# Kernel tuning notes

Measured on AMD Instinct MI355X. Metric: run time of the kernel, lower is better.

Reference implementation:

```python
import jax, jax.numpy as jnp
import numpy as np

B, N, F = 4, 3000, 128

def setup_inputs() -> dict:
    key = jax.random.key(0)
    k1, k2, k3, k4 = jax.random.split(key, 4)
    x = jax.random.normal(k1, (B, N, F), dtype=jnp.float32)
    adj = jax.random.uniform(k2, (B, N, N), dtype=jnp.float32)
    h0 = jax.random.normal(k3, (B, N, F), dtype=jnp.float32)
    stdv = 1.0 / np.sqrt(F)
    theta = jax.random.uniform(k4, (F, F), dtype=jnp.float32, minval=-stdv, maxval=stdv)
    return {
        "x": x, "adj": adj, "h0": h0, "theta": theta,
        "lamda": jnp.float32(0.5), "alpha": jnp.float32(0.1), "l": 4,
    }

def _normalize_adj(adj):
    # add self loops, then D^{-1/2} A D^{-1/2} via elementwise row/col scaling
    # (same math as diag-embed + inverse + two bmms in the original)
    n = adj.shape[1]
    adj = adj + jnp.eye(n, dtype=adj.dtype)
    deg = jnp.sum(adj, axis=2)                      # [B, N]
    d_inv_sqrt = jax.lax.rsqrt(deg)                 # [B, N]
    return d_inv_sqrt[:, :, None] * adj * d_inv_sqrt[:, None, :]

def reference(x, adj, h0, theta, lamda, alpha, l):
    adj_n = _normalize_adj(adj)
    beta = jnp.log(lamda / l + 1.0)
    hi = jnp.einsum('bnm,bmf->bnf', adj_n, x)       # aggregation
    support = (1.0 - alpha) * hi + alpha * h0       # variant=False path
    r = support
    out = beta * jnp.einsum('bnf,fg->bng', support, theta) + (1.0 - beta) * r
    return out
```

## Files before the change

kernel.cpp:

```cpp
#include <hip/hip_runtime.h>
#include <hip/hip_bf16.h>
#include <math.h>

#define BB 4
#define NN 3000
#define FF 128
#define NKC 96
#define NIT 188
#define TS  532

typedef __bf16 bf16x8 __attribute__((ext_vector_type(8)));
typedef __bf16 bf16x4 __attribute__((ext_vector_type(4)));
typedef __bf16 bf16x8a __attribute__((ext_vector_type(8), aligned(8)));
typedef __bf16 bf16x4a __attribute__((ext_vector_type(4), aligned(4)));
typedef float  f32x4  __attribute__((ext_vector_type(4)));


__global__ __launch_bounds__(256) void k_degpk(const float* __restrict__ adj,
                                               float* __restrict__ dis,
                                               __bf16* __restrict__ apk) {
    const int b = blockIdx.y, it = blockIdx.x;
    const int i0 = it * 16;
    const int t = threadIdx.x, w = t >> 6, l = t & 63;
    const int m = l & 15, q = l >> 4;
    const int irow = i0 + m;
    const bool rv = irow < NN;
    const float* arow = adj + ((size_t)b * NN + irow) * NN;
    __bf16* apt = apk + ((size_t)(b * NIT + it) * NKC) * 512 + l * 8;

    float rsum = 0.f;
    for (int kc = w; kc < NKC; kc += 4) {
        int c0 = kc * 32 + q * 8;
        float4 u = {0.f, 0.f, 0.f, 0.f}, v = {0.f, 0.f, 0.f, 0.f};
        if (rv && c0 + 8 <= NN) {
            u = *(const float4*)(arow + c0);
            v = *(const float4*)(arow + c0 + 4);
        }
        rsum += (u.x + u.y) + (u.z + u.w) + (v.x + v.y) + (v.z + v.w);
        bf16x8 s;
        s[0] = (__bf16)u.x; s[1] = (__bf16)u.y; s[2] = (__bf16)u.z; s[3] = (__bf16)u.w;
        s[4] = (__bf16)v.x; s[5] = (__bf16)v.y; s[6] = (__bf16)v.z; s[7] = (__bf16)v.w;
        *(bf16x8*)(apt + (size_t)kc * 512) = s;
    }
    rsum += __shfl_xor(rsum, 16, 64);
    rsum += __shfl_xor(rsum, 32, 64);
    __shared__ float ssum[4][16];
    if (q == 0) ssum[w][m] = rsum;
    __syncthreads();
    if (t < 16 && i0 + t < NN) {
        float tot = ssum[0][t] + ssum[1][t] + ssum[2][t] + ssum[3][t] + 1.0f;
        dis[b * NN + i0 + t] = 1.0f / sqrtf(tot);
    }
}

__global__ __launch_bounds__(256) void k_aggs(const __bf16* __restrict__ apk,
                                              const __bf16* __restrict__ xpk,
                                              const __bf16* __restrict__ thpk,
                                              const float* __restrict__ x,
                                              const float* __restrict__ h0,
                                              const float* __restrict__ dis,
                                              float* __restrict__ out,
                                              const float* __restrict__ alpha_p,
                                              const float* __restrict__ lamda_p,
                                              const int* __restrict__ l_p) {
    __shared__ __bf16 stile[16][140];
    const int id = blockIdx.x;
    const int b  = (id >> 1) & 3;
    const int it = (id >> 3) * 2 + (id & 1);
    const int i0 = it * 16;
    const int t  = threadIdx.x, w = t >> 6, l = t & 63;
    const int m  = l & 15, quad = l >> 4;
    const int n0 = w * 32;
    const __bf16* A0 = apk + ((size_t)(b * NIT + it) * NKC) * 512 + l * 8;
    const __bf16* B0 = xpk + ((size_t)(b * 8 + 2 * w) * NKC) * 512 + l * 8;
    const __bf16* B1 = B0 + (size_t)NKC * 512;
    f32x4 acc0 = {0.f, 0.f, 0.f, 0.f};
    f32x4 acc1 = {0.f, 0.f, 0.f, 0.f};

    #pragma unroll 8
    for (int kc = 0; kc < NKC; ++kc) {
        bf16x8 a  = *(const bf16x8*)(A0 + (size_t)kc * 512);
        bf16x8 b0 = *(const bf16x8*)(B0 + (size_t)kc * 512);
        bf16x8 b1 = *(const bf16x8*)(B1 + (size_t)kc * 512);
        acc0 = __builtin_amdgcn_mfma_f32_16x16x32_bf16(a, b0, acc0, 0, 0, 0);
        acc1 = __builtin_amdgcn_mfma_f32_16x16x32_bf16(a, b1, acc1, 0, 0, 0);
    }

    const float alpha = *alpha_p;
    const float beta  = logf(*lamda_p / (float)(*l_p) + 1.0f);
    float s0v[4], s1v[4];
    #pragma unroll
    for (int r = 0; r < 4; ++r) {
        int row  = quad * 4 + r;
        int irow = i0 + row;
        float s0 = 0.f, s1 = 0.f;
        if (irow < NN) {
            float  di   = dis[b * NN + irow];
            size_t base = ((size_t)b * NN + irow) * FF;
            int c0 = n0 + m, c1 = n0 + 16 + m;
            s0 = (1.f - alpha) * (di * acc0[r] + di * di * x[base + c0]) + alpha * h0[base + c0];
            s1 = (1.f - alpha) * (di * acc1[r] + di * di * x[base + c1]) + alpha * h0[base + c1];
        }
        s0v[r] = s0; s1v[r] = s1;
        stile[row][n0 + m]      = (__bf16)s0;
        stile[row][n0 + 16 + m] = (__bf16)s1;
    }
    __syncthreads();
    f32x4 o0 = {0.f, 0.f, 0.f, 0.f};
    f32x4 o1 = {0.f, 0.f, 0.f, 0.f};
    const __bf16* T0 = thpk + (size_t)(2 * w * 4) * 512 + l * 8;
    const __bf16* T1 = T0 + 4 * 512;
    #pragma unroll
    for (int kc = 0; kc < 4; ++kc) {
        bf16x4a alo = *(const bf16x4a*)&stile[m][kc * 32 + quad * 8];
        bf16x4a ahi = *(const bf16x4a*)&stile[m][kc * 32 + quad * 8 + 4];
        bf16x8 a = __builtin_shufflevector(alo, ahi, 0, 1, 2, 3, 4, 5, 6, 7);
        bf16x8 tb0 = *(const bf16x8*)(T0 + (size_t)kc * 512);
        bf16x8 tb1 = *(const bf16x8*)(T1 + (size_t)kc * 512);
        o0 = __builtin_amdgcn_mfma_f32_16x16x32_bf16(a, tb0, o0, 0, 0, 0);
        o1 = __builtin_amdgcn_mfma_f32_16x16x32_bf16(a, tb1, o1, 0, 0, 0);
    }
    const float omb = 1.f - beta;
    #pragma unroll
    for (int r = 0; r < 4; ++r) {
        int irow = i0 + quad * 4 + r;
        if (irow < NN) {
            size_t base = ((size_t)b * NN + irow) * FF;
            out[base + n0 + m]      = beta * o0[r] + omb * s0v[r];
            out[base + n0 + 16 + m] = beta * o1[r] + omb * s1v[r];
        }
    }
}


__global__ __launch_bounds__(256) void k_xpk(const float* __restrict__ x,
                                             const float* __restrict__ dis,
                                             __bf16* __restrict__ xpk) {
    int b  = blockIdx.y, kc = blockIdx.x;
    int t  = threadIdx.x, w = t >> 6, l = t & 63;
    int m  = l & 15, q = l >> 4;
    #pragma unroll
    for (int h = 0; h < 2; ++h) {
        int nt = w + h * 4;
        int f  = nt * 16 + m;
        bf16x8 v;
        #pragma unroll
        for (int j = 0; j < 8; ++j) {
            int k = kc * 32 + q * 8 + j;
            float val = 0.f;
            if (k < NN) val = dis[b * NN + k] * x[((size_t)b * NN + k) * FF + f];
            v[j] = (__bf16)val;
        }
        *(bf16x8*)(xpk + ((size_t)(b * 8 + nt) * NKC + kc) * 512 + l * 8) = v;
    }
}

__global__ __launch_bounds__(256) void k_thpk(const float* __restrict__ theta,
                                              __bf16* __restrict__ thpk) {
    int kc = blockIdx.x;
    int t  = threadIdx.x, w = t >> 6, l = t & 63;
    int m  = l & 15, q = l >> 4;
    #pragma unroll
    for (int h = 0; h < 2; ++h) {
        int nt = w + h * 4;
        bf16x8 v;
        #pragma unroll
        for (int j = 0; j < 8; ++j) {
            int k = kc * 32 + q * 8 + j;
            v[j] = (__bf16)theta[k * FF + nt * 16 + m];
        }
        *(bf16x8*)(thpk + ((size_t)(nt * 4 + kc)) * 512 + l * 8) = v;
    }
}


__global__ __launch_bounds__(256) void k_deg(const float* __restrict__ adj,
                                             float* __restrict__ dis) {
    int wid  = (blockIdx.x * 256 + threadIdx.x) >> 6;
    int lane = threadIdx.x & 63;
    if (wid >= BB * NN) return;
    const float4* row = (const float4*)(adj + (size_t)wid * NN);
    float s = 0.f;
    for (int c = lane; c < NN / 4; c += 64) {
        float4 v = row[c];
        s += (v.x + v.y) + (v.z + v.w);
    }
    for (int off = 32; off > 0; off >>= 1) s += __shfl_down(s, off, 64);
    if (lane == 0) dis[wid] = 1.0f / sqrtf(s + 1.0f);
}

__global__ __launch_bounds__(256) void k_agg(const float* __restrict__ adj,
                                             const __bf16* __restrict__ xpk,
                                             const __bf16* __restrict__ thpk,
                                             const float* __restrict__ x,
                                             const float* __restrict__ h0,
                                             const float* __restrict__ dis,
                                             float* __restrict__ out,
                                             const float* __restrict__ alpha_p,
                                             const float* __restrict__ lamda_p,
                                             const int* __restrict__ l_p) {
    __shared__ __bf16 tile[2][16][TS];
    __shared__ __bf16 stile[16][140];
    const int id = blockIdx.x;
    const int b  = (id >> 1) & 3;
    const int it = (id >> 3) * 2 + (id & 1);
    const int i0 = it * 16;
    const int t  = threadIdx.x, w = t >> 6, l = t & 63;
    const int m  = l & 15, quad = l >> 4;
    const int n0 = w * 32;
    const __bf16* B0 = xpk + ((size_t)(b * 8 + 2 * w) * NKC) * 512 + l * 8;
    const __bf16* B1 = B0 + (size_t)NKC * 512;
    f32x4 acc0 = {0.f, 0.f, 0.f, 0.f};
    f32x4 acc1 = {0.f, 0.f, 0.f, 0.f};

    float4 pu[4], pv[4];
    auto load_chunk = [&](int c) {
        #pragma unroll
        for (int i = 0; i < 4; ++i) {
            int row  = i * 4 + w;
            int irow = i0 + row;
            int col  = c * 512 + l * 8;
            float4 u = {0.f, 0.f, 0.f, 0.f}, v = {0.f, 0.f, 0.f, 0.f};
            if (irow < NN && col < NN) {
                const float* p = adj + ((size_t)b * NN + irow) * NN + col;
                u = *(const float4*)p;
                v = *(const float4*)(p + 4);
            }
            pu[i] = u; pv[i] = v;
        }
    };
    auto store_chunk = [&](int cb) {
        #pragma unroll
        for (int i = 0; i < 4; ++i) {
            int row = i * 4 + w;
            bf16x8a s;
            s[0] = (__bf16)pu[i].x; s[1] = (__bf16)pu[i].y;
            s[2] = (__bf16)pu[i].z; s[3] = (__bf16)pu[i].w;
            s[4] = (__bf16)pv[i].x; s[5] = (__bf16)pv[i].y;
            s[6] = (__bf16)pv[i].z; s[7] = (__bf16)pv[i].w;
            *(bf16x8a*)&tile[cb][row][l * 8] = s;
        }
    };

    load_chunk(0);
    store_chunk(0);
    __syncthreads();
    for (int c = 0; c < 6; ++c) {
        int cb = c & 1;
        if (c < 5) load_chunk(c + 1);
        #pragma unroll 4
        for (int kcl = 0; kcl < 16; ++kcl) {
            int kc = c * 16 + kcl;
            bf16x8 a = *(const bf16x8a*)&tile[cb][m][kcl * 32 + quad * 8];
            bf16x8 b0 = *(const bf16x8*)(B0 + (size_t)kc * 512);
            bf16x8 b1 = *(const bf16x8*)(B1 + (size_t)kc * 512);
            acc0 = __builtin_amdgcn_mfma_f32_16x16x32_bf16(a, b0, acc0, 0, 0, 0);
            acc1 = __builtin_amdgcn_mfma_f32_16x16x32_bf16(a, b1, acc1, 0, 0, 0);
        }
        if (c < 5) store_chunk(cb ^ 1);
        __syncthreads();
    }

    const float alpha = *alpha_p;
    const float beta  = logf(*lamda_p / (float)(*l_p) + 1.0f);
    float s0v[4], s1v[4];
    #pragma unroll
    for (int r = 0; r < 4; ++r) {
        int row  = quad * 4 + r;
        int irow = i0 + row;
        float s0 = 0.f, s1 = 0.f;
        if (irow < NN) {
            float  di   = dis[b * NN + irow];
            size_t base = ((size_t)b * NN + irow) * FF;
            int c0 = n0 + m, c1 = n0 + 16 + m;
            s0 = (1.f - alpha) * (di * acc0[r] + di * di * x[base + c0]) + alpha * h0[base + c0];
            s1 = (1.f - alpha) * (di * acc1[r] + di * di * x[base + c1]) + alpha * h0[base + c1];
        }
        s0v[r] = s0; s1v[r] = s1;
        stile[row][n0 + m]      = (__bf16)s0;
        stile[row][n0 + 16 + m] = (__bf16)s1;
    }
    __syncthreads();
    f32x4 o0 = {0.f, 0.f, 0.f, 0.f};
    f32x4 o1 = {0.f, 0.f, 0.f, 0.f};
    const __bf16* T0 = thpk + (size_t)(2 * w * 4) * 512 + l * 8;
    const __bf16* T1 = T0 + 4 * 512;
    #pragma unroll
    for (int kc = 0; kc < 4; ++kc) {
        bf16x4a alo = *(const bf16x4a*)&stile[m][kc * 32 + quad * 8];
        bf16x4a ahi = *(const bf16x4a*)&stile[m][kc * 32 + quad * 8 + 4];
        bf16x8 a = __builtin_shufflevector(alo, ahi, 0, 1, 2, 3, 4, 5, 6, 7);
        bf16x8 tb0 = *(const bf16x8*)(T0 + (size_t)kc * 512);
        bf16x8 tb1 = *(const bf16x8*)(T1 + (size_t)kc * 512);
        o0 = __builtin_amdgcn_mfma_f32_16x16x32_bf16(a, tb0, o0, 0, 0, 0);
        o1 = __builtin_amdgcn_mfma_f32_16x16x32_bf16(a, tb1, o1, 0, 0, 0);
    }
    const float omb = 1.f - beta;
    #pragma unroll
    for (int r = 0; r < 4; ++r) {
        int irow = i0 + quad * 4 + r;
        if (irow < NN) {
            size_t base = ((size_t)b * NN + irow) * FF;
            out[base + n0 + m]      = beta * o0[r] + omb * s0v[r];
            out[base + n0 + 16 + m] = beta * o1[r] + omb * s1v[r];
        }
    }
}


extern "C" void kernel_launch(void* const* d_in, const int* in_sizes, int n_in,
                              void* d_out, int out_size, void* d_ws, size_t ws_size,
                              hipStream_t stream) {
    const float* x      = (const float*)d_in[0];
    const float* adj    = (const float*)d_in[1];
    const float* h0     = (const float*)d_in[2];
    const float* theta  = (const float*)d_in[3];
    const float* lamda  = (const float*)d_in[4];
    const float* alpha  = (const float*)d_in[5];
    const int*   l      = (const int*)d_in[6];
    float* out = (float*)d_out;

    char* ws = (char*)d_ws;

    const size_t APK_OFF  = 3276800;
    const size_t WS_NEED  = APK_OFF + (size_t)BB * NIT * NKC * 512 * 2;

    if (ws_size >= WS_NEED) {
        float*  dis  = (float*)ws;
        __bf16* thpk = (__bf16*)(ws + 65536);
        __bf16* xpk  = (__bf16*)(ws + 131072);
        __bf16* apk  = (__bf16*)(ws + APK_OFF);

        k_degpk<<<dim3(NIT, BB), 256, 0, stream>>>(adj, dis, apk);
        k_thpk<<<dim3(4), 256, 0, stream>>>(theta, thpk);
        k_xpk<<<dim3(NKC, BB), 256, 0, stream>>>(x, dis, xpk);
        k_aggs<<<dim3(NIT * BB), 256, 0, stream>>>(apk, xpk, thpk, x, h0, dis, out,
                                                   alpha, lamda, l);
    } else {
        float*  dis  = (float*)ws;
        __bf16* xpk  = (__bf16*)(ws + 65536);
        __bf16* thpk = (__bf16*)(ws + 3276800);

        k_deg<<<dim3((BB * NN) / 4), 256, 0, stream>>>(adj, dis);
        k_thpk<<<dim3(4), 256, 0, stream>>>(theta, thpk);
        k_xpk<<<dim3(NKC, BB), 256, 0, stream>>>(x, dis, xpk);
        k_agg<<<dim3(NIT * BB), 256, 0, stream>>>(adj, xpk, thpk, x, h0, dis, out,
                                                  alpha, lamda, l);
    }
}
```

Before: 284.1 us.

## Store bf16 adjacency row-major padded and fuse theta packing into x packing

The degree-and-convert kernel now uses one wavefront per adjacency row. It streams the row with fully coalesced float4 reads and writes a padded row-major bf16 copy (3008x3072 per batch) instead of the MFMA-tiled packed layout. The aggregation kernel reads its A fragments directly from this row-major buffer, with 16-byte loads strided by row. The theta packing kernel is folded into the x packing kernel to drop one launch. This makes the adjacency conversion pass cheaper to read, but the GEMM's A loads become less contiguous per wavefront. It also relies on the unwritten padding rows being harmless.

```diff
diff --git a/kernel.cpp b/kernel.cpp
--- a/kernel.cpp
+++ b/kernel.cpp
@@ -4,10 +4,11 @@
 
 #define BB 4
 #define NN 3000
+#define NR 3008
+#define NC 3072
 #define FF 128
 #define NKC 96
 #define NIT 188
-#define TS  532
 
 typedef __bf16 bf16x8 __attribute__((ext_vector_type(8)));
 typedef __bf16 bf16x4 __attribute__((ext_vector_type(4)));
@@ -15,54 +16,76 @@
 typedef __bf16 bf16x4a __attribute__((ext_vector_type(4), aligned(4)));
 typedef float  f32x4  __attribute__((ext_vector_type(4)));
 
-
-__global__ __launch_bounds__(256) void k_degpk(const float* __restrict__ adj,
-                                               float* __restrict__ dis,
-                                               __bf16* __restrict__ apk) {
-    const int b = blockIdx.y, it = blockIdx.x;
-    const int i0 = it * 16;
-    const int t = threadIdx.x, w = t >> 6, l = t & 63;
-    const int m = l & 15, q = l >> 4;
-    const int irow = i0 + m;
-    const bool rv = irow < NN;
-    const float* arow = adj + ((size_t)b * NN + irow) * NN;
-    __bf16* apt = apk + ((size_t)(b * NIT + it) * NKC) * 512 + l * 8;
-
-    float rsum = 0.f;
-    for (int kc = w; kc < NKC; kc += 4) {
-        int c0 = kc * 32 + q * 8;
-        float4 u = {0.f, 0.f, 0.f, 0.f}, v = {0.f, 0.f, 0.f, 0.f};
-        if (rv && c0 + 8 <= NN) {
-            u = *(const float4*)(arow + c0);
-            v = *(const float4*)(arow + c0 + 4);
-        }
-        rsum += (u.x + u.y) + (u.z + u.w) + (v.x + v.y) + (v.z + v.w);
-        bf16x8 s;
-        s[0] = (__bf16)u.x; s[1] = (__bf16)u.y; s[2] = (__bf16)u.z; s[3] = (__bf16)u.w;
-        s[4] = (__bf16)v.x; s[5] = (__bf16)v.y; s[6] = (__bf16)v.z; s[7] = (__bf16)v.w;
-        *(bf16x8*)(apt + (size_t)kc * 512) = s;
-    }
-    rsum += __shfl_xor(rsum, 16, 64);
-    rsum += __shfl_xor(rsum, 32, 64);
-    __shared__ float ssum[4][16];
-    if (q == 0) ssum[w][m] = rsum;
-    __syncthreads();
-    if (t < 16 && i0 + t < NN) {
-        float tot = ssum[0][t] + ssum[1][t] + ssum[2][t] + ssum[3][t] + 1.0f;
-        dis[b * NN + i0 + t] = 1.0f / sqrtf(tot);
-    }
-}
-
-__global__ __launch_bounds__(256) void k_aggs(const __bf16* __restrict__ apk,
-                                              const __bf16* __restrict__ xpk,
-                                              const __bf16* __restrict__ thpk,
-                                              const float* __restrict__ x,
-                                              const float* __restrict__ h0,
-                                              const float* __restrict__ dis,
-                                              float* __restrict__ out,
-                                              const float* __restrict__ alpha_p,
-                                              const float* __restrict__ lamda_p,
-                                              const int* __restrict__ l_p) {
+__global__ __launch_bounds__(256) void k_degpk2(const float* __restrict__ adj,
+                                                float* __restrict__ dis,
+                                                __bf16* __restrict__ apk) {
+    int wid  = (blockIdx.x * 256 + threadIdx.x) >> 6;
+    int lane = threadIdx.x & 63;
+    if (wid >= BB * NN) return;
+    int b = wid / NN, i = wid - b * NN;
+    const float4* row4 = (const float4*)(adj + (size_t)wid * NN);
+    __bf16* prow = apk + ((size_t)b * NR + i) * NC;
+    float s = 0.f;
+    for (int c = lane; c < 768; c += 64) {
+        float4 v = {0.f, 0.f, 0.f, 0.f};
+        if (c < 750) v = row4[c];
+        s += (v.x + v.y) + (v.z + v.w);
+        bf16x4a o;
+        o[0] = (__bf16)v.x; o[1] = (__bf16)v.y;
+        o[2] = (__bf16)v.z; o[3] = (__bf16)v.w;
+        *(bf16x4a*)(prow + c * 4) = o;
+    }
+    for (int off = 32; off > 0; off >>= 1) s += __shfl_down(s, off, 64);
+    if (lane == 0) dis[wid] = 1.0f / sqrtf(s + 1.0f);
+}
+
+__global__ __launch_bounds__(256) void k_xpk(const float* __restrict__ x,
+                                             const float* __restrict__ dis,
+                                             const float* __restrict__ theta,
+                                             __bf16* __restrict__ xpk,
+                                             __bf16* __restrict__ thpk) {
+    int b  = blockIdx.y, kc = blockIdx.x;
+    int t  = threadIdx.x, w = t >> 6, l = t & 63;
+    int m  = l & 15, q = l >> 4;
+    #pragma unroll
+    for (int h = 0; h < 2; ++h) {
+        int nt = w + h * 4;
+        int f  = nt * 16 + m;
+        bf16x8 v;
+        #pragma unroll
+        for (int j = 0; j < 8; ++j) {
+            int k = kc * 32 + q * 8 + j;
+            float val = 0.f;
+            if (k < NN) val = dis[b * NN + k] * x[((size_t)b * NN + k) * FF + f];
+            v[j] = (__bf16)val;
+        }
+        *(bf16x8*)(xpk + ((size_t)(b * 8 + nt) * NKC + kc) * 512 + l * 8) = v;
+    }
+    if (b == 0 && kc < 4) {
+        #pragma unroll
+        for (int h = 0; h < 2; ++h) {
+            int nt = w + h * 4;
+            bf16x8 v;
+            #pragma unroll
+            for (int j = 0; j < 8; ++j) {
+                int k = kc * 32 + q * 8 + j;
+                v[j] = (__bf16)theta[k * FF + nt * 16 + m];
+            }
+            *(bf16x8*)(thpk + ((size_t)(nt * 4 + kc)) * 512 + l * 8) = v;
+        }
+    }
+}
+
+__global__ __launch_bounds__(256) void k_aggs2(const __bf16* __restrict__ apk,
+                                               const __bf16* __restrict__ xpk,
+                                               const __bf16* __restrict__ thpk,
+                                               const float* __restrict__ x,
+                                               const float* __restrict__ h0,
+                                               const float* __restrict__ dis,
+                                               float* __restrict__ out,
+                                               const float* __restrict__ alpha_p,
+                                               const float* __restrict__ lamda_p,
+                                               const int* __restrict__ l_p) {
     __shared__ __bf16 stile[16][140];
     const int id = blockIdx.x;
     const int b  = (id >> 1) & 3;
@@ -71,7 +94,7 @@
     const int t  = threadIdx.x, w = t >> 6, l = t & 63;
     const int m  = l & 15, quad = l >> 4;
     const int n0 = w * 32;
-    const __bf16* A0 = apk + ((size_t)(b * NIT + it) * NKC) * 512 + l * 8;
+    const __bf16* A0 = apk + ((size_t)b * NR + (i0 + m)) * NC + quad * 8;
     const __bf16* B0 = xpk + ((size_t)(b * 8 + 2 * w) * NKC) * 512 + l * 8;
     const __bf16* B1 = B0 + (size_t)NKC * 512;
     f32x4 acc0 = {0.f, 0.f, 0.f, 0.f};
@@ -79,7 +102,7 @@
 
     #pragma unroll 8
     for (int kc = 0; kc < NKC; ++kc) {
-        bf16x8 a  = *(const bf16x8*)(A0 + (size_t)kc * 512);
+        bf16x8 a  = *(const bf16x8*)(A0 + kc * 32);
         bf16x8 b0 = *(const bf16x8*)(B0 + (size_t)kc * 512);
         bf16x8 b1 = *(const bf16x8*)(B1 + (size_t)kc * 512);
         acc0 = __builtin_amdgcn_mfma_f32_16x16x32_bf16(a, b0, acc0, 0, 0, 0);
@@ -132,48 +155,7 @@
     }
 }
 
-
-__global__ __launch_bounds__(256) void k_xpk(const float* __restrict__ x,
-                                             const float* __restrict__ dis,
-                                             __bf16* __restrict__ xpk) {
-    int b  = blockIdx.y, kc = blockIdx.x;
-    int t  = threadIdx.x, w = t >> 6, l = t & 63;
-    int m  = l & 15, q = l >> 4;
-    #pragma unroll
-    for (int h = 0; h < 2; ++h) {
-        int nt = w + h * 4;
-        int f  = nt * 16 + m;
-        bf16x8 v;
-        #pragma unroll
-        for (int j = 0; j < 8; ++j) {
-            int k = kc * 32 + q * 8 + j;
-            float val = 0.f;
-            if (k < NN) val = dis[b * NN + k] * x[((size_t)b * NN + k) * FF + f];
-            v[j] = (__bf16)val;
-        }
-        *(bf16x8*)(xpk + ((size_t)(b * 8 + nt) * NKC + kc) * 512 + l * 8) = v;
-    }
-}
-
-__global__ __launch_bounds__(256) void k_thpk(const float* __restrict__ theta,
-                                              __bf16* __restrict__ thpk) {
-    int kc = blockIdx.x;
-    int t  = threadIdx.x, w = t >> 6, l = t & 63;
-    int m  = l & 15, q = l >> 4;
-    #pragma unroll
-    for (int h = 0; h < 2; ++h) {
-        int nt = w + h * 4;
-        bf16x8 v;
-        #pragma unroll
-        for (int j = 0; j < 8; ++j) {
-            int k = kc * 32 + q * 8 + j;
-            v[j] = (__bf16)theta[k * FF + nt * 16 + m];
-        }
-        *(bf16x8*)(thpk + ((size_t)(nt * 4 + kc)) * 512 + l * 8) = v;
-    }
-}
-
-
+#define TS 532
 __global__ __launch_bounds__(256) void k_deg(const float* __restrict__ adj,
                                              float* __restrict__ dis) {
     int wid  = (blockIdx.x * 256 + threadIdx.x) >> 6;
@@ -307,6 +289,46 @@
     }
 }
 
+__global__ __launch_bounds__(256) void k_thpk_fb(const float* __restrict__ theta,
+                                                 __bf16* __restrict__ thpk) {
+    int kc = blockIdx.x;
+    int t  = threadIdx.x, w = t >> 6, l = t & 63;
+    int m  = l & 15, q = l >> 4;
+    #pragma unroll
+    for (int h = 0; h < 2; ++h) {
+        int nt = w + h * 4;
+        bf16x8 v;
+        #pragma unroll
+        for (int j = 0; j < 8; ++j) {
+            int k = kc * 32 + q * 8 + j;
+            v[j] = (__bf16)theta[k * FF + nt * 16 + m];
+        }
+        *(bf16x8*)(thpk + ((size_t)(nt * 4 + kc)) * 512 + l * 8) = v;
+    }
+}
+
+__global__ __launch_bounds__(256) void k_xpk_fb(const float* __restrict__ x,
+                                                const float* __restrict__ dis,
+                                                __bf16* __restrict__ xpk) {
+    int b  = blockIdx.y, kc = blockIdx.x;
+    int t  = threadIdx.x, w = t >> 6, l = t & 63;
+    int m  = l & 15, q = l >> 4;
+    #pragma unroll
+    for (int h = 0; h < 2; ++h) {
+        int nt = w + h * 4;
+        int f  = nt * 16 + m;
+        bf16x8 v;
+        #pragma unroll
+        for (int j = 0; j < 8; ++j) {
+            int k = kc * 32 + q * 8 + j;
+            float val = 0.f;
+            if (k < NN) val = dis[b * NN + k] * x[((size_t)b * NN + k) * FF + f];
+            v[j] = (__bf16)val;
+        }
+        *(bf16x8*)(xpk + ((size_t)(b * 8 + nt) * NKC + kc) * 512 + l * 8) = v;
+    }
+}
+
 
 extern "C" void kernel_launch(void* const* d_in, const int* in_sizes, int n_in,
                               void* d_out, int out_size, void* d_ws, size_t ws_size,
@@ -322,8 +344,8 @@
 
     char* ws = (char*)d_ws;
 
-    const size_t APK_OFF  = 3276800;
-    const size_t WS_NEED  = APK_OFF + (size_t)BB * NIT * NKC * 512 * 2;
+    const size_t APK_OFF = 3276800;
+    const size_t WS_NEED = APK_OFF + (size_t)BB * NR * NC * 2;
 
     if (ws_size >= WS_NEED) {
         float*  dis  = (float*)ws;
@@ -331,19 +353,18 @@
         __bf16* xpk  = (__bf16*)(ws + 131072);
         __bf16* apk  = (__bf16*)(ws + APK_OFF);
 
-        k_degpk<<<dim3(NIT, BB), 256, 0, stream>>>(adj, dis, apk);
-        k_thpk<<<dim3(4), 256, 0, stream>>>(theta, thpk);
-        k_xpk<<<dim3(NKC, BB), 256, 0, stream>>>(x, dis, xpk);
-        k_aggs<<<dim3(NIT * BB), 256, 0, stream>>>(apk, xpk, thpk, x, h0, dis, out,
-                                                   alpha, lamda, l);
+        k_degpk2<<<dim3((BB * NN) / 4), 256, 0, stream>>>(adj, dis, apk);
+        k_xpk<<<dim3(NKC, BB), 256, 0, stream>>>(x, dis, theta, xpk, thpk);
+        k_aggs2<<<dim3(NIT * BB), 256, 0, stream>>>(apk, xpk, thpk, x, h0, dis, out,
+                                                    alpha, lamda, l);
     } else {
         float*  dis  = (float*)ws;
         __bf16* xpk  = (__bf16*)(ws + 65536);
         __bf16* thpk = (__bf16*)(ws + 3276800);
 
         k_deg<<<dim3((BB * NN) / 4), 256, 0, stream>>>(adj, dis);
-        k_thpk<<<dim3(4), 256, 0, stream>>>(theta, thpk);
-        k_xpk<<<dim3(NKC, BB), 256, 0, stream>>>(x, dis, xpk);
+        k_thpk_fb<<<dim3(4), 256, 0, stream>>>(theta, thpk);
+        k_xpk_fb<<<dim3(NKC, BB), 256, 0, stream>>>(x, dis, xpk);
         k_agg<<<dim3(NIT * BB), 256, 0, stream>>>(adj, xpk, thpk, x, h0, dis, out,
                                                   alpha, lamda, l);
     }
```

Result: slower. 305.6 us (+7.6%).
